# Performance work log

Hardware: AMD Instinct MI355X
Metric: run time of the kernel (lower is better)

Reference implementation:

```python
import jax, jax.numpy as jnp
import numpy as np

B, N, H, L, V = 512, 20, 450, 56, 780
T = 2 * (N - 1)  # DFS trace length per tree (down+up edge per non-root node)


def _build(rng):
    EpT = 2 * (N - 1)
    n_nodes, n_edges = B * N, B * EpT
    src = np.zeros(n_edges, np.int32); dst = np.zeros(n_edges, np.int32)
    step_eid = np.zeros((T, B), np.int32)
    step_v = np.zeros((T, B), np.int32)
    p_flag = np.zeros((T, B), np.int32)
    for b in range(B):
        par = [0] * N
        ch = [[] for _ in range(N)]
        for i in range(1, N):
            p = int(rng.integers(max(0, i - 3), i))
            par[i] = p; ch[p].append(i)
        eo, no = b * EpT, b * N
        for i in range(1, N):
            d, u = eo + 2 * (i - 1), eo + 2 * (i - 1) + 1
            src[d], dst[d] = no + par[i], no + i
            src[u], dst[u] = no + i, no + par[i]
        trace = []
        stack = [(0, iter(ch[0]))]
        while stack:
            u_, it = stack[-1]
            c = next(it, None)
            if c is None:
                stack.pop()
                if stack:
                    pu = stack[-1][0]
                    trace.append((eo + 2 * (u_ - 1) + 1, no + pu, 0))
            else:
                trace.append((eo + 2 * (c - 1), no + c, 1))
                stack.append((c, iter(ch[c])))
        for t, (e, v, p) in enumerate(trace):
            step_eid[t, b], step_v[t, b], p_flag[t, b] = e, v, p
    return src, dst, step_eid, step_v, p_flag


def setup_inputs() -> dict:
    rng = np.random.default_rng(0)
    src, dst, step_eid, step_v, p_flag = _build(rng)
    n_nodes, n_edges = B * N, B * 2 * (N - 1)
    in_lists = [[] for _ in range(n_nodes)]
    for e in range(n_edges):
        in_lists[dst[e]].append(e)
    Dn = max(len(l) for l in in_lists)
    node_in = np.full((n_nodes, Dn), n_edges, np.int32)  # pad with sentinel n_edges
    for v, l in enumerate(in_lists):
        node_in[v, :len(l)] = l
    # line-graph (non-backtracking) predecessors of edge e=(u,v): edges (w,u), w != v
    preds = [[e2 for e2 in in_lists[src[e]] if src[e2] != dst[e]] for e in range(n_edges)]
    P = max(1, max(len(l) for l in preds))
    edge_pred = np.full((n_edges, P), n_edges, np.int32)
    for e, l in enumerate(preds):
        edge_pred[e, :len(l)] = l
    wid = rng.integers(0, V, n_nodes).astype(np.int32)
    root_ids = (np.arange(B) * N).astype(np.int32)
    # q rows: root block, then per-step rows where node is new (down edges)
    q_rows = list(range(B)); q_tgt = [int(wid[r]) for r in root_ids]
    for t in range(T):
        for b in range(B):
            if p_flag[t, b]:
                q_rows.append((t + 1) * B + b)
                q_tgt.append(int(wid[step_v[t, b]]))
    p_tgt = np.concatenate([p_flag.reshape(-1), np.zeros(B, np.int32)]).astype(np.int32)
    key = jax.random.key(0)
    def W(k, *shape):
        return jax.random.normal(jax.random.fold_in(key, k), shape, jnp.float32) * 0.05
    return dict(
        tree_vec=W(0, B, L), emb=W(1, V, H),
        Wz=W(2, 2 * H, H), bz=jnp.zeros(H, jnp.float32),
        Wh=W(3, 2 * H, H), bh=jnp.zeros(H, jnp.float32),
        Wr=W(4, H, H), Ur=W(5, H, H), br=jnp.zeros(H, jnp.float32),
        Ww=W(6, H + L, H), bw=jnp.zeros(H, jnp.float32),
        Uw=W(7, 2 * H + L, H), bu=jnp.zeros(H, jnp.float32),
        Wo=W(8, H, V), bo=jnp.zeros(V, jnp.float32),
        Us=W(9, H, 1), bs=jnp.zeros(1, jnp.float32),
        wid=jnp.asarray(wid), root_ids=jnp.asarray(root_ids),
        edge_src=jnp.asarray(src), edge_dst=jnp.asarray(dst),
        edge_pred=jnp.asarray(edge_pred), node_in=jnp.asarray(node_in),
        step_eid=jnp.asarray(step_eid), step_v=jnp.asarray(step_v),
        q_rows=jnp.asarray(np.array(q_rows, np.int32)),
        q_tgt=jnp.asarray(np.array(q_tgt, np.int32)),
        p_tgt=jnp.asarray(p_tgt),
    )


def reference(tree_vec, emb, Wz, bz, Wh, bh, Wr, Ur, br, Ww, bw, Uw, bu, Wo, bo, Us, bs,
              wid, root_ids, edge_src, edge_dst, edge_pred, node_in, step_eid, step_v,
              q_rows, q_tgt, p_tgt):
    n_edges = edge_src.shape[0]
    x = emb[wid]                              # [n_nodes, H] node embeddings
    src_x = x[edge_src]; dst_x = x[edge_dst]  # [n_edges, H]
    m0 = jnp.zeros((n_edges + 1, H), x.dtype)  # +1 sentinel zero row for padding

    def step(carry, inp):
        m, rm = carry
        eid, v = inp                          # [B] edge ids / dst node ids this DFS step
        pred = edge_pred[eid]                 # [B, P] non-backtracking predecessor edges
        s = m[pred].sum(1)                    # sum of incoming m
        arm = rm[pred].sum(1)                 # sum of incoming r*m
        sx = src_x[eid]; dx = dst_x[eid]
        z = jax.nn.sigmoid(jnp.concatenate([sx, s], 1) @ Wz + bz)
        m_new = (1 - z) * s + z * jnp.tanh(jnp.concatenate([sx, arm], 1) @ Wh + bh)
        r = jax.nn.sigmoid(dx @ Wr + m_new @ Ur + br)
        m = m.at[eid].set(m_new)
        rm = rm.at[eid].set(r * m_new)
        h = m[node_in[v]].sum(1)              # node pull: h_v = sum of incoming m
        return (m, rm), h

    _, h_steps = jax.lax.scan(step, (m0, m0), (step_eid, step_v))  # [T, B, H]

    x_root = x[root_ids]
    h_root = jnp.zeros_like(x_root)           # roots pulled before any edge update
    x_steps = x[step_v]                        # [T, B, H]
    tv_steps = jnp.broadcast_to(tree_vec[None], (T, B, L))
    p_root = jnp.concatenate([x_root, h_root, tree_vec], 1)[None]
    p_step = jnp.concatenate([x_steps, h_steps, tv_steps], 2)
    p_in = jnp.concatenate([p_root, p_step], 0).reshape((T + 1) * B, 2 * H + L)
    q_root = jnp.concatenate([h_root, tree_vec], 1)[None]
    q_step = jnp.concatenate([h_steps, tv_steps], 2)
    q_in = jnp.concatenate([q_root, q_step], 0).reshape((T + 1) * B, H + L)[q_rows]

    q_logits = jax.nn.relu(q_in @ Ww + bw) @ Wo + bo          # [nq, V]
    p_logit = (jax.nn.relu(p_in @ Uw + bu) @ Us + bs)[:, 0]   # [np]
    tgt = p_tgt.astype(p_logit.dtype)
    p_loss = jnp.sum(jnp.logaddexp(0.0, p_logit) - p_logit * tgt) / B
    lse = jax.nn.logsumexp(q_logits, axis=1)
    q_loss = jnp.sum(lse - jnp.take_along_axis(q_logits, q_tgt[:, None], 1)[:, 0]) / B
    p_acc = jnp.mean(((p_logit > 0).astype(p_tgt.dtype) == p_tgt).astype(jnp.float32))
    q_acc = jnp.mean((jnp.argmax(q_logits, 1).astype(q_tgt.dtype) == q_tgt).astype(jnp.float32))
    return (q_loss, p_loss, q_acc, p_acc)
```

## Files before the change

### kernel.cpp

```cpp
#include <hip/hip_runtime.h>
#include <math.h>

#define B_ 512
#define N_ 20
#define H_ 450
#define L_ 56
#define V_ 780
#define T_ 38
#define NNODES (B_*N_)
#define NEDGES (B_*2*(N_-1))
#define NPROWS ((T_+1)*B_)
#define KS 480
#define NT 2
#define AST 488
#define HSTR 456
#define KQ 512
#define KPP 992
#define LDL 784

typedef __attribute__((ext_vector_type(8))) short bf16x8;
typedef __attribute__((ext_vector_type(4))) float f32x4;

__device__ __forceinline__ float sigmoidf_(float v){ return 1.0f/(1.0f+expf(-v)); }

__device__ __forceinline__ unsigned short f2b(float x){
  unsigned int u = __float_as_uint(x);
  unsigned int r = (u + 0x7fffu + ((u >> 16) & 1u)) >> 16;
  return (unsigned short)r;
}
__device__ __forceinline__ float b2f(unsigned int v){
  return __uint_as_float((v & 0xffffu) << 16);
}
__device__ __forceinline__ unsigned int pack2(float lo, float hi){
  return (unsigned int)f2b(lo) | ((unsigned int)f2b(hi) << 16);
}

__global__ __launch_bounds__(256) void k_gather_xb(const float* __restrict__ emb,
    const int* __restrict__ wid, unsigned short* __restrict__ xb){
  int w = blockIdx.x*4 + (threadIdx.x>>6), lane = threadIdx.x & 63;
  if (w >= NNODES) return;
  const float2* src = (const float2*)(emb + (size_t)wid[w]*H_);
  unsigned int* dst = (unsigned int*)(xb + (size_t)w*KS);
  for (int j2 = lane; j2 < 240; j2 += 64){
    unsigned int v = 0;
    if (j2 < 225){ float2 f = src[j2]; v = pack2(f.x, f.y); }
    dst[j2] = v;
  }
}

__global__ void k_wtall(const float* __restrict__ Wz, const float* __restrict__ Wh,
    const float* __restrict__ Ur, const float* __restrict__ Wr,
    const float* __restrict__ Ww, const float* __restrict__ Uw,
    const float* __restrict__ Wo, const float* __restrict__ tv,
    unsigned short* __restrict__ WzB, unsigned short* __restrict__ WhB,
    unsigned short* __restrict__ UrT, unsigned short* __restrict__ WzTop,
    unsigned short* __restrict__ WhTop, unsigned short* __restrict__ WrT,
    unsigned short* __restrict__ WwT, unsigned short* __restrict__ UwT,
    unsigned short* __restrict__ WoT, unsigned short* __restrict__ tvb){
  int bid = blockIdx.x;
  if (bid < 512*6){
    int seg = bid >> 9, c = bid & 511;
    const float* src; unsigned short* dst; int rowbase;
    switch(seg){
      case 0: src = Wz; dst = WzB; rowbase = 450; break;
      case 1: src = Wh; dst = WhB; rowbase = 450; break;
      case 2: src = Ur; dst = UrT; rowbase = 0; break;
      case 3: src = Wz; dst = WzTop; rowbase = 0; break;
      case 4: src = Wh; dst = WhTop; rowbase = 0; break;
      default: src = Wr; dst = WrT; rowbase = 0; break;
    }
    unsigned short* drow = dst + (size_t)c*KS;
    for (int k = threadIdx.x; k < KS; k += blockDim.x){
      float v = 0.f;
      if (c < 450 && k < 450) v = src[(size_t)(rowbase + k)*450 + c];
      drow[k] = f2b(v);
    }
  } else if (bid < 512*7){
    int c = bid - 512*6;
    unsigned short* drow = WwT + (size_t)c*KQ;
    for (int k = threadIdx.x; k < KQ; k += blockDim.x){
      float v = 0.f;
      if (c < 450){
        if (k < 450) v = Ww[(size_t)k*450 + c];
        else if (k >= 456) v = Ww[(size_t)(450 + k - 456)*450 + c];
      }
      drow[k] = f2b(v);
    }
  } else if (bid < 512*8){
    int c = bid - 512*7;
    unsigned short* drow = UwT + (size_t)c*KPP;
    for (int k = threadIdx.x; k < KPP; k += blockDim.x){
      float v = 0.f;
      if (c < 450){
        if (k < 450) v = Uw[(size_t)k*450 + c];
        else if (k >= 480 && k < 930) v = Uw[(size_t)(450 + k - 480)*450 + c];
        else if (k >= 936) v = Uw[(size_t)(900 + k - 936)*450 + c];
      }
      drow[k] = f2b(v);
    }
  } else if (bid < 512*8 + 832){
    int c = bid - 512*8;
    unsigned short* drow = WoT + (size_t)c*512;
    for (int k = threadIdx.x; k < 512; k += blockDim.x){
      float v = 0.f;
      if (c < V_ && k < 450) v = Wo[(size_t)k*V_ + c];
      drow[k] = f2b(v);
    }
  } else {
    int b = bid - (512*8 + 832);
    unsigned short* drow = tvb + (size_t)b*64;
    for (int k = threadIdx.x; k < 64; k += blockDim.x)
      drow[k] = f2b((k < L_) ? tv[b*L_ + k] : 0.f);
  }
}

struct ScanP {
  const unsigned short *WzB, *WhB, *UrT;
  const unsigned short *XWz, *XWh, *XWr;
  const int *edge_src, *edge_dst, *step_eid;
  unsigned short *m, *rm;
  unsigned short *hm, *hrm;
  unsigned short *hb;
};

__global__ __launch_bounds__(1024, 4) void k_scan_tree(ScanP p){
  __shared__ unsigned short A1s[16*AST];
  __shared__ unsigned short A2s[16*AST];
  __shared__ unsigned short A3s[16*AST];
  __shared__ unsigned short sZ[NT*HSTR], sH[NT*HSTR], sR[NT*HSTR];
  __shared__ int s_eoff[T_][NT], s_roff[T_][NT], s_srcH[T_][NT], s_dstH[T_][NT];

  const int tid = threadIdx.x;
  const int lane = tid & 63, l15 = lane & 15, kh = lane >> 4, ko = kh*8;
  const int wv = tid >> 6;
  const int r0 = blockIdx.x * NT;
  const int c_0 = wv*32 + l15, c_1 = c_0 + 16;

  const unsigned short* pWz0 = p.WzB + (size_t)c_0*KS;
  const unsigned short* pWz1 = p.WzB + (size_t)c_1*KS;
  const unsigned short* pWh0 = p.WhB + (size_t)c_0*KS;
  const unsigned short* pWh1 = p.WhB + (size_t)c_1*KS;
  const unsigned short* pUr0 = p.UrT + (size_t)c_0*KS;
  const unsigned short* pUr1 = p.UrT + (size_t)c_1*KS;
  const unsigned short* aA1 = A1s + l15*AST;
  const unsigned short* aA2 = A2s + l15*AST;
  const unsigned short* aA3 = A3s + l15*AST;

  for (int idx = tid; idx < 16*AST; idx += 1024){ A1s[idx] = 0; A2s[idx] = 0; A3s[idx] = 0; }
  for (int idx = tid; idx < T_*NT; idx += 1024){
    int t = idx / NT, rl = idx % NT;
    int e = p.step_eid[t*B_ + r0 + rl];
    s_eoff[t][rl] = e*KS;
    s_roff[t][rl] = (e ^ 1)*KS;
    s_srcH[t][rl] = p.edge_src[e]*HSTR;
    s_dstH[t][rl] = p.edge_dst[e]*HSTR;
  }
  __syncthreads();

  for (int t = 0; t < T_; ++t){
    bf16x8 bz0[3], bz1[3], bh0[3], bh1[3];
    #pragma unroll
    for (int i = 0; i < 3; ++i){
      bz0[i] = *(const bf16x8*)(pWz0 + i*32 + ko);
      bz1[i] = *(const bf16x8*)(pWz1 + i*32 + ko);
      bh0[i] = *(const bf16x8*)(pWh0 + i*32 + ko);
      bh1[i] = *(const bf16x8*)(pWh1 + i*32 + ko);
    }

    if (tid < NT*57){
      int rl = tid / 57, g = tid - rl*57;
      int j = g*8;
      uint4 hm4 = *(const uint4*)(p.hm  + s_srcH[t][rl] + j);
      uint4 hr4 = *(const uint4*)(p.hrm + s_srcH[t][rl] + j);
      uint4 mr4 = *(const uint4*)(p.m   + s_roff[t][rl] + j);
      uint4 rr4 = *(const uint4*)(p.rm  + s_roff[t][rl] + j);
      uint4 o1, o2;
      o1.x = pack2(b2f(hm4.x)-b2f(mr4.x), b2f(hm4.x>>16)-b2f(mr4.x>>16));
      o1.y = pack2(b2f(hm4.y)-b2f(mr4.y), b2f(hm4.y>>16)-b2f(mr4.y>>16));
      o1.z = pack2(b2f(hm4.z)-b2f(mr4.z), b2f(hm4.z>>16)-b2f(mr4.z>>16));
      o1.w = pack2(b2f(hm4.w)-b2f(mr4.w), b2f(hm4.w>>16)-b2f(mr4.w>>16));
      o2.x = pack2(b2f(hr4.x)-b2f(rr4.x), b2f(hr4.x>>16)-b2f(rr4.x>>16));
      o2.y = pack2(b2f(hr4.y)-b2f(rr4.y), b2f(hr4.y>>16)-b2f(rr4.y>>16));
      o2.z = pack2(b2f(hr4.z)-b2f(rr4.z), b2f(hr4.z>>16)-b2f(rr4.z>>16));
      o2.w = pack2(b2f(hr4.w)-b2f(rr4.w), b2f(hr4.w>>16)-b2f(rr4.w>>16));
      *(uint4*)(A1s + rl*AST + j) = o1;
      *(uint4*)(A2s + rl*AST + j) = o2;
    } else if (tid >= 128 && tid < 128 + 3*NT*57){
      int idx2 = tid - 128;
      int mat = idx2 / (NT*57), rem = idx2 - mat*(NT*57);
      int rl = rem / 57, g = rem - rl*57;
      int row = (mat == 2) ? s_dstH[t][rl] : s_srcH[t][rl];
      const unsigned short* src = (mat == 0) ? p.XWz : (mat == 1) ? p.XWh : p.XWr;
      unsigned short* d = (mat == 0) ? sZ : (mat == 1) ? sH : sR;
      *(uint4*)(d + rl*HSTR + g*8) = *(const uint4*)(src + row + g*8);
    }
    __syncthreads();

    f32x4 accZ0 = {}, accZ1 = {}, accH0 = {}, accH1 = {};
    #pragma unroll
    for (int it = 0; it < 15; ++it){
      const int sl = it % 3;
      bf16x8 a1 = *(const bf16x8*)(aA1 + it*32 + ko);
      bf16x8 a2 = *(const bf16x8*)(aA2 + it*32 + ko);
      accZ0 = __builtin_amdgcn_mfma_f32_16x16x32_bf16(a1, bz0[sl], accZ0, 0,0,0);
      accZ1 = __builtin_amdgcn_mfma_f32_16x16x32_bf16(a1, bz1[sl], accZ1, 0,0,0);
      accH0 = __builtin_amdgcn_mfma_f32_16x16x32_bf16(a2, bh0[sl], accH0, 0,0,0);
      accH1 = __builtin_amdgcn_mfma_f32_16x16x32_bf16(a2, bh1[sl], accH1, 0,0,0);
      if (it + 3 < 15){
        bz0[sl] = *(const bf16x8*)(pWz0 + (it+3)*32 + ko);
        bz1[sl] = *(const bf16x8*)(pWz1 + (it+3)*32 + ko);
        bh0[sl] = *(const bf16x8*)(pWh0 + (it+3)*32 + ko);
        bh1[sl] = *(const bf16x8*)(pWh1 + (it+3)*32 + ko);
      }
    }

    bf16x8 bu0[3], bu1[3];
    #pragma unroll
    for (int i = 0; i < 3; ++i){
      bu0[i] = *(const bf16x8*)(pUr0 + i*32 + ko);
      bu1[i] = *(const bf16x8*)(pUr1 + i*32 + ko);
    }

    if (kh == 0){
      #pragma unroll
      for (int n = 0; n < 2; ++n){
        int cc = wv*32 + n*16 + l15;
        if (cc < H_){
          f32x4 aZ = n ? accZ1 : accZ0;
          f32x4 aH = n ? accH1 : accH0;
          #pragma unroll
          for (int reg = 0; reg < NT; ++reg){
            int rl = reg;
            float z  = sigmoidf_(aZ[reg] + b2f(sZ[rl*HSTR + cc]));
            float th = tanhf   (aH[reg] + b2f(sH[rl*HSTR + cc]));
            float s_ = b2f(A1s[rl*AST + cc]);
            float mn = (1.f - z)*s_ + z*th;
            unsigned short mb = f2b(mn);
            p.m[s_eoff[t][rl] + cc] = mb;
            A3s[rl*AST + cc] = mb;
            float hv = b2f(p.hm[s_dstH[t][rl] + cc]) + mn;
            p.hm[s_dstH[t][rl] + cc] = f2b(hv);
            p.hb[(size_t)(t*B_ + r0 + rl)*HSTR + cc] = f2b(hv);
          }
        }
      }
    }
    __syncthreads();

    f32x4 accR0 = {}, accR1 = {};
    #pragma unroll
    for (int it = 0; it < 15; ++it){
      const int sl = it % 3;
      bf16x8 a = *(const bf16x8*)(aA3 + it*32 + ko);
      accR0 = __builtin_amdgcn_mfma_f32_16x16x32_bf16(a, bu0[sl], accR0, 0,0,0);
      accR1 = __builtin_amdgcn_mfma_f32_16x16x32_bf16(a, bu1[sl], accR1, 0,0,0);
      if (it + 3 < 15){
        bu0[sl] = *(const bf16x8*)(pUr0 + (it+3)*32 + ko);
        bu1[sl] = *(const bf16x8*)(pUr1 + (it+3)*32 + ko);
      }
    }

    if (kh == 0){
      #pragma unroll
      for (int n = 0; n < 2; ++n){
        int cc = wv*32 + n*16 + l15;
        if (cc < H_){
          f32x4 aR = n ? accR1 : accR0;
          #pragma unroll
          for (int reg = 0; reg < NT; ++reg){
            int rl = reg;
            float r_ = sigmoidf_(aR[reg] + b2f(sR[rl*HSTR + cc]));
            float mn = b2f(A3s[rl*AST + cc]);
            float rv = r_*mn;
            p.rm[s_eoff[t][rl] + cc] = f2b(rv);
            float hv = b2f(p.hrm[s_dstH[t][rl] + cc]) + rv;
            p.hrm[s_dstH[t][rl] + cc] = f2b(hv);
          }
        }
      }
    }
    __syncthreads();
  }
}

__global__ __launch_bounds__(256) void k_head_mfma(
    const unsigned short* __restrict__ A, const unsigned short* __restrict__ BT, int K,
    const float* __restrict__ bias, int Nact, int relu,
    float* __restrict__ outF, int ldF, unsigned short* __restrict__ outB, int ldB)
{
  __shared__ unsigned short As[64*40], Bs[64*40];
  const int tid = threadIdx.x;
  const int gr0 = blockIdx.y*64, gc0 = blockIdx.x*64;
  const int lane = tid & 63;
  const int w = tid >> 6, wr = w >> 1, wc = w & 1;
  const int l15 = lane & 15, kh = lane >> 4;
  const int sr = tid >> 2, sj = (tid & 3) * 8;
  f32x4 acc[2][2] = {};
  for (int kt = 0; kt < K; kt += 32){
    __syncthreads();
    *(float4*)&As[sr*40 + sj] = *(const float4*)&A[(size_t)(gr0+sr)*K + kt + sj];
    *(float4*)&Bs[sr*40 + sj] = *(const float4*)&BT[(size_t)(gc0+sr)*K + kt + sj];
    __syncthreads();
    bf16x8 a0 = *(const bf16x8*)&As[(wr*32      + l15)*40 + kh*8];
    bf16x8 a1 = *(const bf16x8*)&As[(wr*32 + 16 + l15)*40 + kh*8];
    bf16x8 b0 = *(const bf16x8*)&Bs[(wc*32      + l15)*40 + kh*8];
    bf16x8 b1 = *(const bf16x8*)&Bs[(wc*32 + 16 + l15)*40 + kh*8];
    acc[0][0] = __builtin_amdgcn_mfma_f32_16x16x32_bf16(a0,b0,acc[0][0],0,0,0);
    acc[0][1] = __builtin_amdgcn_mfma_f32_16x16x32_bf16(a0,b1,acc[0][1],0,0,0);
    acc[1][0] = __builtin_amdgcn_mfma_f32_16x16x32_bf16(a1,b0,acc[1][0],0,0,0);
    acc[1][1] = __builtin_amdgcn_mfma_f32_16x16x32_bf16(a1,b1,acc[1][1],0,0,0);
  }
  #pragma unroll
  for (int mi = 0; mi < 2; ++mi){
    #pragma unroll
    for (int n = 0; n < 2; ++n){
      int c = gc0 + wc*32 + n*16 + l15;
      float bc = (c < Nact) ? bias[c] : 0.f;
      #pragma unroll
      for (int reg = 0; reg < 4; ++reg){
        int r = gr0 + wr*32 + mi*16 + kh*4 + reg;
        float v = acc[mi][n][reg] + bc;
        if (relu) v = fmaxf(v, 0.f);
        if (outF && c < Nact) outF[(size_t)r*ldF + c] = v;
        if (outB && c < ldB)  outB[(size_t)r*ldB + c] = (c < Nact) ? f2b(v) : (unsigned short)0;
      }
    }
  }
}

__global__ __launch_bounds__(256) void k_xw(const unsigned short* __restrict__ xb,
    const unsigned short* __restrict__ WzTop, const unsigned short* __restrict__ WhTop,
    const unsigned short* __restrict__ WrT,
    const float* __restrict__ bz, const float* __restrict__ bh, const float* __restrict__ br,
    unsigned short* __restrict__ XWz, unsigned short* __restrict__ XWh,
    unsigned short* __restrict__ XWr)
{
  __shared__ unsigned short As[64*40], Bs[64*40];
  const unsigned short* BT = (blockIdx.z == 0) ? WzTop : (blockIdx.z == 1) ? WhTop : WrT;
  const float* bias        = (blockIdx.z == 0) ? bz    : (blockIdx.z == 1) ? bh    : br;
  unsigned short* outB     = (blockIdx.z == 0) ? XWz   : (blockIdx.z == 1) ? XWh   : XWr;
  const int tid = threadIdx.x;
  const int gr0 = blockIdx.y*64, gc0 = blockIdx.x*64;
  const int lane = tid & 63;
  const int w = tid >> 6, wr = w >> 1, wc = w & 1;
  const int l15 = lane & 15, kh = lane >> 4;
  const int sr = tid >> 2, sj = (tid & 3) * 8;
  f32x4 acc[2][2] = {};
  for (int kt = 0; kt < KS; kt += 32){
    __syncthreads();
    *(float4*)&As[sr*40 + sj] = *(const float4*)&xb[(size_t)(gr0+sr)*KS + kt + sj];
    *(float4*)&Bs[sr*40 + sj] = *(const float4*)&BT[(size_t)(gc0+sr)*KS + kt + sj];
    __syncthreads();
    bf16x8 a0 = *(const bf16x8*)&As[(wr*32      + l15)*40 + kh*8];
    bf16x8 a1 = *(const bf16x8*)&As[(wr*32 + 16 + l15)*40 + kh*8];
    bf16x8 b0 = *(const bf16x8*)&Bs[(wc*32      + l15)*40 + kh*8];
// ... 183 lines not shown
      int tg = q_tgt[i];
      float lt = b2f((unsigned int)logits[(size_t)i*LDL + tg]);
      qloss += mx + logf(ps) - lt;
      qacc  += (mi == tg) ? 1.f : 0.f;
    }
  }
  if (lane == 0){
    atomicAdd(out+0, qloss*(1.0f/B_));
    atomicAdd(out+2, qacc *(1.0f/(float)nq));
  }
}

__global__ __launch_bounds__(256) void k_pfinal(const float* __restrict__ plog,
    const float* __restrict__ bs, const int* __restrict__ p_tgt, float* __restrict__ out){
  int i = blockIdx.x*256 + threadIdx.x;
  float loss = 0.f, acc = 0.f;
  if (i < NPROWS){
    float pl = plog[i] + bs[0];
    float tgt = (float)p_tgt[i];
    loss = fmaxf(pl, 0.f) + log1pf(expf(-fabsf(pl))) - pl*tgt;
    acc = (((pl > 0.f) ? 1 : 0) == p_tgt[i]) ? 1.f : 0.f;
  }
  #pragma unroll
  for (int off = 32; off; off >>= 1){
    loss += __shfl_xor(loss, off); acc += __shfl_xor(acc, off);
  }
  if ((threadIdx.x & 63) == 0){
    atomicAdd(out+1, loss*(1.0f/B_));
    atomicAdd(out+3, acc *(1.0f/(float)NPROWS));
  }
}

extern "C" void kernel_launch(void* const* d_in, const int* in_sizes, int n_in,
                              void* d_out, int out_size, void* d_ws, size_t ws_size,
                              hipStream_t stream){
  const float* tree_vec = (const float*)d_in[0];
  const float* emb  = (const float*)d_in[1];
  const float* Wz   = (const float*)d_in[2];
  const float* bz   = (const float*)d_in[3];
  const float* Wh   = (const float*)d_in[4];
  const float* bh   = (const float*)d_in[5];
  const float* Wr   = (const float*)d_in[6];
  const float* Ur   = (const float*)d_in[7];
  const float* br   = (const float*)d_in[8];
  const float* Ww   = (const float*)d_in[9];
  const float* bw   = (const float*)d_in[10];
  const float* Uw   = (const float*)d_in[11];
  const float* bu   = (const float*)d_in[12];
  const float* Wo   = (const float*)d_in[13];
  const float* bo   = (const float*)d_in[14];
  const float* Us   = (const float*)d_in[15];
  const float* bs   = (const float*)d_in[16];
  const int* wid      = (const int*)d_in[17];
  const int* root_ids = (const int*)d_in[18];
  const int* edge_src = (const int*)d_in[19];
  const int* edge_dst = (const int*)d_in[20];
  const int* step_eid = (const int*)d_in[23];
  const int* step_v   = (const int*)d_in[24];
  const int* q_rows   = (const int*)d_in[25];
  const int* q_tgt    = (const int*)d_in[26];
  const int* p_tgt    = (const int*)d_in[27];
  int nq = in_sizes[25];

  char* ws = (char*)d_ws;
  const size_t XB_OFF    = 0;
  const size_t HB_OFF    = 9830400;
  const size_t M_OFF     = 27574272;
  const size_t RM_OFF    = M_OFF + 18678784;
  const size_t HM_OFF    = RM_OFF + 18678784;
  const size_t HRM_OFF   = HM_OFF + 9338880;
  const size_t WZB_OFF   = HRM_OFF + 9338880;
  const size_t WHB_OFF   = WZB_OFF + 491520;
  const size_t URT_OFF   = WHB_OFF + 491520;
  const size_t WZTOP_OFF = URT_OFF + 491520;
  const size_t WHTOP_OFF = WZTOP_OFF + 491520;
  const size_t WRT_OFF   = WHTOP_OFF + 491520;
  const size_t WWT_OFF   = WRT_OFF + 491520;
  const size_t UWT_OFF   = WWT_OFF + 524288;
  const size_t WOT_OFF   = UWT_OFF + 1015808;
  const size_t TVB_OFF   = WOT_OFF + 851968;
  const size_t XWZ_OFF   = TVB_OFF + 65536;
  const size_t XWH_OFF   = XWZ_OFF + 9338880;
  const size_t XWR_OFF   = XWH_OFF + 9338880;
  const size_t LQ_OFF  = M_OFF;
  const size_t HQB_OFF = XWZ_OFF;
  const size_t PL_OFF  = XWH_OFF;

  unsigned short* xb = (unsigned short*)(ws + XB_OFF);
  unsigned short* hb = (unsigned short*)(ws + HB_OFF);
  unsigned short* m_ = (unsigned short*)(ws + M_OFF);
  unsigned short* rm = (unsigned short*)(ws + RM_OFF);
  unsigned short* hm = (unsigned short*)(ws + HM_OFF);
  unsigned short* hrm = (unsigned short*)(ws + HRM_OFF);
  unsigned short* WzB = (unsigned short*)(ws + WZB_OFF);
  unsigned short* WhB = (unsigned short*)(ws + WHB_OFF);
  unsigned short* UrT = (unsigned short*)(ws + URT_OFF);
  unsigned short* WzTop = (unsigned short*)(ws + WZTOP_OFF);
  unsigned short* WhTop = (unsigned short*)(ws + WHTOP_OFF);
  unsigned short* WrT = (unsigned short*)(ws + WRT_OFF);
  unsigned short* WwT = (unsigned short*)(ws + WWT_OFF);
  unsigned short* UwT = (unsigned short*)(ws + UWT_OFF);
  unsigned short* WoT = (unsigned short*)(ws + WOT_OFF);
  unsigned short* tvb = (unsigned short*)(ws + TVB_OFF);
  unsigned short* XWz = (unsigned short*)(ws + XWZ_OFF);
  unsigned short* XWh = (unsigned short*)(ws + XWH_OFF);
  unsigned short* XWr = (unsigned short*)(ws + XWR_OFF);

  hipMemsetAsync(ws + M_OFF, 0, 2*18678784ull + 2*9338880ull, stream);
  hipMemsetAsync(d_out, 0, (size_t)out_size*sizeof(float), stream);

  k_gather_xb<<<2560, 256, 0, stream>>>(emb, wid, xb);
  k_wtall<<<512*8 + 832 + 512, 256, 0, stream>>>(Wz, Wh, Ur, Wr, Ww, Uw, Wo, tree_vec,
      WzB, WhB, UrT, WzTop, WhTop, WrT, WwT, UwT, WoT, tvb);
  k_xw<<<dim3(8,160,3), 256, 0, stream>>>(xb, WzTop, WhTop, WrT, bz, bh, br, XWz, XWh, XWr);

  ScanP sp;
  sp.WzB = WzB; sp.WhB = WhB; sp.UrT = UrT;
  sp.XWz = XWz; sp.XWh = XWh; sp.XWr = XWr;
  sp.edge_src = edge_src; sp.edge_dst = edge_dst; sp.step_eid = step_eid;
  sp.m = m_; sp.rm = rm; sp.hm = hm; sp.hrm = hrm; sp.hb = hb;
  k_scan_tree<<<B_/NT, 1024, 0, stream>>>(sp);

  unsigned short* logitsq = (unsigned short*)(ws + LQ_OFF);
  unsigned short* hqb     = (unsigned short*)(ws + HQB_OFF);
  float* plog             = (float*)(ws + PL_OFF);
  hipMemsetAsync(plog, 0, (size_t)NPROWS*4, stream);

  k_head_q<<<dim3(8, nq/64), 256, 0, stream>>>(hb, tvb, q_rows, WwT, bw, hqb, nq);
  k_head_mfma<<<dim3(13, nq/64), 256, 0, stream>>>(hqb, WoT, 512, bo, V_, 0,
      nullptr, 0, logitsq, LDL);
  k_qreduce3<<<320, 256, 0, stream>>>(logitsq, q_tgt, nq, (float*)d_out);

  k_head_p2<<<dim3(8, NPROWS/64), 256, 0, stream>>>(xb, hb, tvb, root_ids, step_v,
      UwT, bu, Us, plog);
  k_pfinal<<<78, 256, 0, stream>>>(plog, bs, p_tgt, (float*)d_out);
}
```

Baseline: 1.200 ms.

## Swizzle LDS A-tiles, split gather across more threads, skip idle wave

Pads the LDS A-tile row stride to 512 and XOR-swizzles column offsets by row, so the MFMA A-fragment reads avoid bank conflicts. The hm/m gather now uses 228 threads with 8-byte loads instead of 114 threads with 16-byte loads, and the XW row copy moves to threads starting at 256. The 16th wave, whose columns fall past H, no longer loads weights or issues MFMAs. The swizzle must match in the writer and every reader, and padded rows that stay zero depend on where the XOR lands.

```diff
diff --git a/kernel.cpp b/kernel.cpp
--- a/kernel.cpp
+++ b/kernel.cpp
@@ -12,7 +12,7 @@
 #define NPROWS ((T_+1)*B_)
 #define KS 480
 #define NT 2
-#define AST 488
+#define AST 512
 #define HSTR 456
 #define KQ 512
 #define KPP 992
@@ -135,6 +135,8 @@
   const int wv = tid >> 6;
   const int r0 = blockIdx.x * NT;
   const int c_0 = wv*32 + l15, c_1 = c_0 + 16;
+  const int sw = (l15 & 7) << 3;
+  const bool act = (wv < 15);
 
   const unsigned short* pWz0 = p.WzB + (size_t)c_0*KS;
   const unsigned short* pWz1 = p.WzB + (size_t)c_1*KS;
@@ -159,34 +161,33 @@
 
   for (int t = 0; t < T_; ++t){
     bf16x8 bz0[3], bz1[3], bh0[3], bh1[3];
-    #pragma unroll
-    for (int i = 0; i < 3; ++i){
-      bz0[i] = *(const bf16x8*)(pWz0 + i*32 + ko);
-      bz1[i] = *(const bf16x8*)(pWz1 + i*32 + ko);
-      bh0[i] = *(const bf16x8*)(pWh0 + i*32 + ko);
-      bh1[i] = *(const bf16x8*)(pWh1 + i*32 + ko);
-    }
-
-    if (tid < NT*57){
-      int rl = tid / 57, g = tid - rl*57;
-      int j = g*8;
-      uint4 hm4 = *(const uint4*)(p.hm  + s_srcH[t][rl] + j);
-      uint4 hr4 = *(const uint4*)(p.hrm + s_srcH[t][rl] + j);
-      uint4 mr4 = *(const uint4*)(p.m   + s_roff[t][rl] + j);
-      uint4 rr4 = *(const uint4*)(p.rm  + s_roff[t][rl] + j);
-      uint4 o1, o2;
-      o1.x = pack2(b2f(hm4.x)-b2f(mr4.x), b2f(hm4.x>>16)-b2f(mr4.x>>16));
-      o1.y = pack2(b2f(hm4.y)-b2f(mr4.y), b2f(hm4.y>>16)-b2f(mr4.y>>16));
-      o1.z = pack2(b2f(hm4.z)-b2f(mr4.z), b2f(hm4.z>>16)-b2f(mr4.z>>16));
-      o1.w = pack2(b2f(hm4.w)-b2f(mr4.w), b2f(hm4.w>>16)-b2f(mr4.w>>16));
-      o2.x = pack2(b2f(hr4.x)-b2f(rr4.x), b2f(hr4.x>>16)-b2f(rr4.x>>16));
-      o2.y = pack2(b2f(hr4.y)-b2f(rr4.y), b2f(hr4.y>>16)-b2f(rr4.y>>16));
-      o2.z = pack2(b2f(hr4.z)-b2f(rr4.z), b2f(hr4.z>>16)-b2f(rr4.z>>16));
-      o2.w = pack2(b2f(hr4.w)-b2f(rr4.w), b2f(hr4.w>>16)-b2f(rr4.w>>16));
-      *(uint4*)(A1s + rl*AST + j) = o1;
-      *(uint4*)(A2s + rl*AST + j) = o2;
-    } else if (tid >= 128 && tid < 128 + 3*NT*57){
-      int idx2 = tid - 128;
+    if (act){
+      #pragma unroll
+      for (int i = 0; i < 3; ++i){
+        bz0[i] = *(const bf16x8*)(pWz0 + i*32 + ko);
+        bz1[i] = *(const bf16x8*)(pWz1 + i*32 + ko);
+        bh0[i] = *(const bf16x8*)(pWh0 + i*32 + ko);
+        bh1[i] = *(const bf16x8*)(pWh1 + i*32 + ko);
+      }
+    }
+
+    if (tid < NT*114){
+      int rl = tid / 114, g = tid - rl*114;
+      int j = g*4;
+      uint2 hm2 = *(const uint2*)(p.hm  + s_srcH[t][rl] + j);
+      uint2 hr2 = *(const uint2*)(p.hrm + s_srcH[t][rl] + j);
+      uint2 mr2 = *(const uint2*)(p.m   + s_roff[t][rl] + j);
+      uint2 rr2 = *(const uint2*)(p.rm  + s_roff[t][rl] + j);
+      uint2 o1, o2;
+      o1.x = pack2(b2f(hm2.x)-b2f(mr2.x), b2f(hm2.x>>16)-b2f(mr2.x>>16));
+      o1.y = pack2(b2f(hm2.y)-b2f(mr2.y), b2f(hm2.y>>16)-b2f(mr2.y>>16));
+      o2.x = pack2(b2f(hr2.x)-b2f(rr2.x), b2f(hr2.x>>16)-b2f(rr2.x>>16));
+      o2.y = pack2(b2f(hr2.y)-b2f(rr2.y), b2f(hr2.y>>16)-b2f(rr2.y>>16));
+      int so = j ^ ((rl & 7) << 3);
+      *(uint2*)(A1s + rl*AST + so) = o1;
+      *(uint2*)(A2s + rl*AST + so) = o2;
+    } else if (tid >= 256 && tid < 256 + 3*NT*57){
+      int idx2 = tid - 256;
       int mat = idx2 / (NT*57), rem = idx2 - mat*(NT*57);
       int rl = rem / 57, g = rem - rl*57;
       int row = (mat == 2) ? s_dstH[t][rl] : s_srcH[t][rl];
@@ -197,28 +198,33 @@
     __syncthreads();
 
     f32x4 accZ0 = {}, accZ1 = {}, accH0 = {}, accH1 = {};
-    #pragma unroll
-    for (int it = 0; it < 15; ++it){
-      const int sl = it % 3;
-      bf16x8 a1 = *(const bf16x8*)(aA1 + it*32 + ko);
-      bf16x8 a2 = *(const bf16x8*)(aA2 + it*32 + ko);
-      accZ0 = __builtin_amdgcn_mfma_f32_16x16x32_bf16(a1, bz0[sl], accZ0, 0,0,0);
-      accZ1 = __builtin_amdgcn_mfma_f32_16x16x32_bf16(a1, bz1[sl], accZ1, 0,0,0);
-      accH0 = __builtin_amdgcn_mfma_f32_16x16x32_bf16(a2, bh0[sl], accH0, 0,0,0);
-      accH1 = __builtin_amdgcn_mfma_f32_16x16x32_bf16(a2, bh1[sl], accH1, 0,0,0);
-      if (it + 3 < 15){
-        bz0[sl] = *(const bf16x8*)(pWz0 + (it+3)*32 + ko);
-        bz1[sl] = *(const bf16x8*)(pWz1 + (it+3)*32 + ko);
-        bh0[sl] = *(const bf16x8*)(pWh0 + (it+3)*32 + ko);
-        bh1[sl] = *(const bf16x8*)(pWh1 + (it+3)*32 + ko);
+    if (act){
+      #pragma unroll
+      for (int it = 0; it < 15; ++it){
+        const int sl = it % 3;
+        const int so = (it*32 + ko) ^ sw;
+        bf16x8 a1 = *(const bf16x8*)(aA1 + so);
+        bf16x8 a2 = *(const bf16x8*)(aA2 + so);
+        accZ0 = __builtin_amdgcn_mfma_f32_16x16x32_bf16(a1, bz0[sl], accZ0, 0,0,0);
+        accZ1 = __builtin_amdgcn_mfma_f32_16x16x32_bf16(a1, bz1[sl], accZ1, 0,0,0);
+        accH0 = __builtin_amdgcn_mfma_f32_16x16x32_bf16(a2, bh0[sl], accH0, 0,0,0);
+        accH1 = __builtin_amdgcn_mfma_f32_16x16x32_bf16(a2, bh1[sl], accH1, 0,0,0);
+        if (it + 3 < 15){
+          bz0[sl] = *(const bf16x8*)(pWz0 + (it+3)*32 + ko);
+          bz1[sl] = *(const bf16x8*)(pWz1 + (it+3)*32 + ko);
+          bh0[sl] = *(const bf16x8*)(pWh0 + (it+3)*32 + ko);
+          bh1[sl] = *(const bf16x8*)(pWh1 + (it+3)*32 + ko);
+        }
       }
     }
 
     bf16x8 bu0[3], bu1[3];
-    #pragma unroll
-    for (int i = 0; i < 3; ++i){
-      bu0[i] = *(const bf16x8*)(pUr0 + i*32 + ko);
-      bu1[i] = *(const bf16x8*)(pUr1 + i*32 + ko);
+    if (act){
+      #pragma unroll
+      for (int i = 0; i < 3; ++i){
+        bu0[i] = *(const bf16x8*)(pUr0 + i*32 + ko);
+        bu1[i] = *(const bf16x8*)(pUr1 + i*32 + ko);
+      }
     }
 
     if (kh == 0){
@@ -231,13 +237,14 @@
           #pragma unroll
           for (int reg = 0; reg < NT; ++reg){
             int rl = reg;
+            int so = cc ^ ((rl & 7) << 3);
             float z  = sigmoidf_(aZ[reg] + b2f(sZ[rl*HSTR + cc]));
             float th = tanhf   (aH[reg] + b2f(sH[rl*HSTR + cc]));
-            float s_ = b2f(A1s[rl*AST + cc]);
+            float s_ = b2f(A1s[rl*AST + so]);
             float mn = (1.f - z)*s_ + z*th;
             unsigned short mb = f2b(mn);
             p.m[s_eoff[t][rl] + cc] = mb;
-            A3s[rl*AST + cc] = mb;
+            A3s[rl*AST + so] = mb;
             float hv = b2f(p.hm[s_dstH[t][rl] + cc]) + mn;
             p.hm[s_dstH[t][rl] + cc] = f2b(hv);
             p.hb[(size_t)(t*B_ + r0 + rl)*HSTR + cc] = f2b(hv);
@@ -248,15 +255,17 @@
     __syncthreads();
 
     f32x4 accR0 = {}, accR1 = {};
-    #pragma unroll
-    for (int it = 0; it < 15; ++it){
-      const int sl = it % 3;
-      bf16x8 a = *(const bf16x8*)(aA3 + it*32 + ko);
-      accR0 = __builtin_amdgcn_mfma_f32_16x16x32_bf16(a, bu0[sl], accR0, 0,0,0);
-      accR1 = __builtin_amdgcn_mfma_f32_16x16x32_bf16(a, bu1[sl], accR1, 0,0,0);
-      if (it + 3 < 15){
-        bu0[sl] = *(const bf16x8*)(pUr0 + (it+3)*32 + ko);
-        bu1[sl] = *(const bf16x8*)(pUr1 + (it+3)*32 + ko);
+    if (act){
+      #pragma unroll
+      for (int it = 0; it < 15; ++it){
+        const int sl = it % 3;
+        bf16x8 a = *(const bf16x8*)(aA3 + ((it*32 + ko) ^ sw));
+        accR0 = __builtin_amdgcn_mfma_f32_16x16x32_bf16(a, bu0[sl], accR0, 0,0,0);
+        accR1 = __builtin_amdgcn_mfma_f32_16x16x32_bf16(a, bu1[sl], accR1, 0,0,0);
+        if (it + 3 < 15){
+          bu0[sl] = *(const bf16x8*)(pUr0 + (it+3)*32 + ko);
+          bu1[sl] = *(const bf16x8*)(pUr1 + (it+3)*32 + ko);
+        }
       }
     }
 
@@ -269,8 +278,9 @@
           #pragma unroll
           for (int reg = 0; reg < NT; ++reg){
             int rl = reg;
+            int so = cc ^ ((rl & 7) << 3);
             float r_ = sigmoidf_(aR[reg] + b2f(sR[rl*HSTR + cc]));
-            float mn = b2f(A3s[rl*AST + cc]);
+            float mn = b2f(A3s[rl*AST + so]);
             float rv = r_*mn;
             p.rm[s_eoff[t][rl] + cc] = f2b(rv);
             float hv = b2f(p.hrm[s_dstH[t][rl] + cc]) + rv;
```

After: 1.554 ms. 1.3x slower.

## Quantize tree-scan recurrent GEMMs to FP8 e4m3 with scaled weights

Applied to the files above, without the earlier changes.

The recurrent matmuls in the sequential tree scan move from bf16 MFMA to fp8 e4m3 MFMA. Weights are pre-quantized with a scale of 16, and activations are quantized to fp8 in shared memory using a permuted layout, which halves weight and LDS traffic per step. A bf16 copy of the message difference is kept for the gating arithmetic. The r-gate now reads m back from global memory instead of shared. This risks accuracy loss from e4m3 rounding of both activations and weights inside a recurrence.

```diff
diff --git a/kernel.cpp b/kernel.cpp
--- a/kernel.cpp
+++ b/kernel.cpp
@@ -12,7 +12,7 @@
 #define NPROWS ((T_+1)*B_)
 #define KS 480
 #define NT 2
-#define AST 488
+#define ASTQ 528
 #define HSTR 456
 #define KQ 512
 #define KPP 992
@@ -20,6 +20,7 @@
 
 typedef __attribute__((ext_vector_type(8))) short bf16x8;
 typedef __attribute__((ext_vector_type(4))) float f32x4;
+typedef __attribute__((ext_vector_type(2))) long i64x2;
 
 __device__ __forceinline__ float sigmoidf_(float v){ return 1.0f/(1.0f+expf(-v)); }
 
@@ -33,6 +34,26 @@
 }
 __device__ __forceinline__ unsigned int pack2(float lo, float hi){
   return (unsigned int)f2b(lo) | ((unsigned int)f2b(hi) << 16);
+}
+__device__ __forceinline__ unsigned char f2e4m3(float x){
+  unsigned int u = __float_as_uint(x);
+  unsigned char sgn = (u >> 24) & 0x80;
+  unsigned int au = u & 0x7fffffffu;
+  if (au >= 0x43e00000u) return sgn | 0x7e;
+  if (au < 0x3c800000u){
+    float t = __uint_as_float(au) * 512.f;
+    int q = (int)rintf(t);
+    if (q >= 8) return sgn | 0x08;
+    return sgn | (unsigned char)q;
+  }
+  unsigned int r = au + 0x7ffffu + ((au >> 20) & 1u);
+  if (r >= 0x43e00000u) return sgn | 0x7e;
+  int e = (int)((r >> 23) & 0xff) - 120;
+  unsigned int m = (r >> 20) & 7u;
+  return sgn | (unsigned char)((e << 3) | m);
+}
+__device__ __forceinline__ int foff_(int k){
+  return ((k >> 3) & 3)*128 + (k >> 5)*8 + (k & 7);
 }
 
 __global__ __launch_bounds__(256) void k_gather_xb(const float* __restrict__ emb,
@@ -114,8 +135,19 @@
   }
 }
 
+__global__ void k_wt8(const float* __restrict__ W, int Kact, int Nact,
+                      unsigned char* __restrict__ dst){
+  int c = blockIdx.x;
+  unsigned char* drow = dst + (size_t)c*512;
+  for (int k = threadIdx.x; k < 512; k += blockDim.x){
+    float v = 0.f;
+    if (c < Nact && k < Kact) v = W[(size_t)k*Nact + c] * 16.f;
+    drow[foff_(k)] = f2e4m3(v);
+  }
+}
+
 struct ScanP {
-  const unsigned short *WzB, *WhB, *UrT;
+  const unsigned char *WzQ, *WhQ, *UrQ;
   const unsigned short *XWz, *XWh, *XWr;
   const int *edge_src, *edge_dst, *step_eid;
   unsigned short *m, *rm;
@@ -124,29 +156,33 @@
 };
 
 __global__ __launch_bounds__(1024, 4) void k_scan_tree(ScanP p){
-  __shared__ unsigned short A1s[16*AST];
-  __shared__ unsigned short A2s[16*AST];
-  __shared__ unsigned short A3s[16*AST];
+  __shared__ unsigned char A1s[16*ASTQ];
+  __shared__ unsigned char A2s[16*ASTQ];
+  __shared__ unsigned char A3s[16*ASTQ];
+  __shared__ unsigned short SLb[NT*HSTR];
   __shared__ unsigned short sZ[NT*HSTR], sH[NT*HSTR], sR[NT*HSTR];
   __shared__ int s_eoff[T_][NT], s_roff[T_][NT], s_srcH[T_][NT], s_dstH[T_][NT];
 
   const int tid = threadIdx.x;
-  const int lane = tid & 63, l15 = lane & 15, kh = lane >> 4, ko = kh*8;
+  const int lane = tid & 63, l15 = lane & 15, kh = lane >> 4;
   const int wv = tid >> 6;
   const int r0 = blockIdx.x * NT;
   const int c_0 = wv*32 + l15, c_1 = c_0 + 16;
 
-  const unsigned short* pWz0 = p.WzB + (size_t)c_0*KS;
-  const unsigned short* pWz1 = p.WzB + (size_t)c_1*KS;
-  const unsigned short* pWh0 = p.WhB + (size_t)c_0*KS;
-  const unsigned short* pWh1 = p.WhB + (size_t)c_1*KS;
-  const unsigned short* pUr0 = p.UrT + (size_t)c_0*KS;
-  const unsigned short* pUr1 = p.UrT + (size_t)c_1*KS;
-  const unsigned short* aA1 = A1s + l15*AST;
-  const unsigned short* aA2 = A2s + l15*AST;
-  const unsigned short* aA3 = A3s + l15*AST;
-
-  for (int idx = tid; idx < 16*AST; idx += 1024){ A1s[idx] = 0; A2s[idx] = 0; A3s[idx] = 0; }
+  const unsigned char* qWz0 = p.WzQ + (size_t)c_0*512 + kh*128;
+  const unsigned char* qWz1 = p.WzQ + (size_t)c_1*512 + kh*128;
+  const unsigned char* qWh0 = p.WhQ + (size_t)c_0*512 + kh*128;
+  const unsigned char* qWh1 = p.WhQ + (size_t)c_1*512 + kh*128;
+  const unsigned char* qUr0 = p.UrQ + (size_t)c_0*512 + kh*128;
+  const unsigned char* qUr1 = p.UrQ + (size_t)c_1*512 + kh*128;
+  const unsigned char* aA1q = A1s + l15*ASTQ + kh*128;
+  const unsigned char* aA2q = A2s + l15*ASTQ + kh*128;
+  const unsigned char* aA3q = A3s + l15*ASTQ + kh*128;
+
+  for (int idx = tid; idx < 16*ASTQ/4; idx += 1024){
+    ((unsigned int*)A1s)[idx] = 0u; ((unsigned int*)A2s)[idx] = 0u;
+    ((unsigned int*)A3s)[idx] = 0u;
+  }
   for (int idx = tid; idx < T_*NT; idx += 1024){
     int t = idx / NT, rl = idx % NT;
     int e = p.step_eid[t*B_ + r0 + rl];
@@ -158,13 +194,13 @@
   __syncthreads();
 
   for (int t = 0; t < T_; ++t){
-    bf16x8 bz0[3], bz1[3], bh0[3], bh1[3];
+    i64x2 rz0[3], rz1[3], rh0[3], rh1[3];
     #pragma unroll
     for (int i = 0; i < 3; ++i){
-      bz0[i] = *(const bf16x8*)(pWz0 + i*32 + ko);
-      bz1[i] = *(const bf16x8*)(pWz1 + i*32 + ko);
-      bh0[i] = *(const bf16x8*)(pWh0 + i*32 + ko);
-      bh1[i] = *(const bf16x8*)(pWh1 + i*32 + ko);
+      rz0[i] = *(const i64x2*)(qWz0 + i*16);
+      rz1[i] = *(const i64x2*)(qWz1 + i*16);
+      rh0[i] = *(const i64x2*)(qWh0 + i*16);
+      rh1[i] = *(const i64x2*)(qWh1 + i*16);
     }
 
     if (tid < NT*57){
@@ -174,17 +210,24 @@
       uint4 hr4 = *(const uint4*)(p.hrm + s_srcH[t][rl] + j);
       uint4 mr4 = *(const uint4*)(p.m   + s_roff[t][rl] + j);
       uint4 rr4 = *(const uint4*)(p.rm  + s_roff[t][rl] + j);
-      uint4 o1, o2;
-      o1.x = pack2(b2f(hm4.x)-b2f(mr4.x), b2f(hm4.x>>16)-b2f(mr4.x>>16));
-      o1.y = pack2(b2f(hm4.y)-b2f(mr4.y), b2f(hm4.y>>16)-b2f(mr4.y>>16));
-      o1.z = pack2(b2f(hm4.z)-b2f(mr4.z), b2f(hm4.z>>16)-b2f(mr4.z>>16));
-      o1.w = pack2(b2f(hm4.w)-b2f(mr4.w), b2f(hm4.w>>16)-b2f(mr4.w>>16));
-      o2.x = pack2(b2f(hr4.x)-b2f(rr4.x), b2f(hr4.x>>16)-b2f(rr4.x>>16));
-      o2.y = pack2(b2f(hr4.y)-b2f(rr4.y), b2f(hr4.y>>16)-b2f(rr4.y>>16));
-      o2.z = pack2(b2f(hr4.z)-b2f(rr4.z), b2f(hr4.z>>16)-b2f(rr4.z>>16));
-      o2.w = pack2(b2f(hr4.w)-b2f(rr4.w), b2f(hr4.w>>16)-b2f(rr4.w>>16));
-      *(uint4*)(A1s + rl*AST + j) = o1;
-      *(uint4*)(A2s + rl*AST + j) = o2;
+      float f0 = b2f(hm4.x)-b2f(mr4.x), f1 = b2f(hm4.x>>16)-b2f(mr4.x>>16);
+      float f2 = b2f(hm4.y)-b2f(mr4.y), f3 = b2f(hm4.y>>16)-b2f(mr4.y>>16);
+      float f4 = b2f(hm4.z)-b2f(mr4.z), f5 = b2f(hm4.z>>16)-b2f(mr4.z>>16);
+      float f6 = b2f(hm4.w)-b2f(mr4.w), f7 = b2f(hm4.w>>16)-b2f(mr4.w>>16);
+      float a0 = b2f(hr4.x)-b2f(rr4.x), a1 = b2f(hr4.x>>16)-b2f(rr4.x>>16);
+      float a2 = b2f(hr4.y)-b2f(rr4.y), a3 = b2f(hr4.y>>16)-b2f(rr4.y>>16);
+      float a4 = b2f(hr4.z)-b2f(rr4.z), a5 = b2f(hr4.z>>16)-b2f(rr4.z>>16);
+      float a6 = b2f(hr4.w)-b2f(rr4.w), a7 = b2f(hr4.w>>16)-b2f(rr4.w>>16);
+      int fo = ((j>>3)&3)*128 + (j>>5)*8;
+      uint2 w1, w2;
+      w1.x = (unsigned)f2e4m3(f0) | ((unsigned)f2e4m3(f1)<<8) | ((unsigned)f2e4m3(f2)<<16) | ((unsigned)f2e4m3(f3)<<24);
+      w1.y = (unsigned)f2e4m3(f4) | ((unsigned)f2e4m3(f5)<<8) | ((unsigned)f2e4m3(f6)<<16) | ((unsigned)f2e4m3(f7)<<24);
+      w2.x = (unsigned)f2e4m3(a0) | ((unsigned)f2e4m3(a1)<<8) | ((unsigned)f2e4m3(a2)<<16) | ((unsigned)f2e4m3(a3)<<24);
+      w2.y = (unsigned)f2e4m3(a4) | ((unsigned)f2e4m3(a5)<<8) | ((unsigned)f2e4m3(a6)<<16) | ((unsigned)f2e4m3(a7)<<24);
+      *(uint2*)(A1s + rl*ASTQ + fo) = w1;
+      *(uint2*)(A2s + rl*ASTQ + fo) = w2;
+      uint4 sb; sb.x = pack2(f0,f1); sb.y = pack2(f2,f3); sb.z = pack2(f4,f5); sb.w = pack2(f6,f7);
+      *(uint4*)(SLb + rl*HSTR + j) = sb;
     } else if (tid >= 128 && tid < 128 + 3*NT*57){
       int idx2 = tid - 128;
       int mat = idx2 / (NT*57), rem = idx2 - mat*(NT*57);
@@ -198,27 +241,31 @@
 
     f32x4 accZ0 = {}, accZ1 = {}, accH0 = {}, accH1 = {};
     #pragma unroll
-    for (int it = 0; it < 15; ++it){
-      const int sl = it % 3;
-      bf16x8 a1 = *(const bf16x8*)(aA1 + it*32 + ko);
-      bf16x8 a2 = *(const bf16x8*)(aA2 + it*32 + ko);
-      accZ0 = __builtin_amdgcn_mfma_f32_16x16x32_bf16(a1, bz0[sl], accZ0, 0,0,0);
-      accZ1 = __builtin_amdgcn_mfma_f32_16x16x32_bf16(a1, bz1[sl], accZ1, 0,0,0);
-      accH0 = __builtin_amdgcn_mfma_f32_16x16x32_bf16(a2, bh0[sl], accH0, 0,0,0);
-      accH1 = __builtin_amdgcn_mfma_f32_16x16x32_bf16(a2, bh1[sl], accH1, 0,0,0);
-      if (it + 3 < 15){
-        bz0[sl] = *(const bf16x8*)(pWz0 + (it+3)*32 + ko);
-        bz1[sl] = *(const bf16x8*)(pWz1 + (it+3)*32 + ko);
-        bh0[sl] = *(const bf16x8*)(pWh0 + (it+3)*32 + ko);
-        bh1[sl] = *(const bf16x8*)(pWh1 + (it+3)*32 + ko);
-      }
-    }
-
-    bf16x8 bu0[3], bu1[3];
+    for (int c = 0; c < 8; ++c){
+      const int sl = c % 3;
+      i64x2 a1 = *(const i64x2*)(aA1q + c*16);
+      i64x2 a2 = *(const i64x2*)(aA2q + c*16);
+      accZ0 = __builtin_amdgcn_mfma_f32_16x16x32_fp8_fp8(a1.x, rz0[sl].x, accZ0, 0,0,0);
+      accZ0 = __builtin_amdgcn_mfma_f32_16x16x32_fp8_fp8(a1.y, rz0[sl].y, accZ0, 0,0,0);
+      accZ1 = __builtin_amdgcn_mfma_f32_16x16x32_fp8_fp8(a1.x, rz1[sl].x, accZ1, 0,0,0);
+      accZ1 = __builtin_amdgcn_mfma_f32_16x16x32_fp8_fp8(a1.y, rz1[sl].y, accZ1, 0,0,0);
+      accH0 = __builtin_amdgcn_mfma_f32_16x16x32_fp8_fp8(a2.x, rh0[sl].x, accH0, 0,0,0);
+      accH0 = __builtin_amdgcn_mfma_f32_16x16x32_fp8_fp8(a2.y, rh0[sl].y, accH0, 0,0,0);
+      accH1 = __builtin_amdgcn_mfma_f32_16x16x32_fp8_fp8(a2.x, rh1[sl].x, accH1, 0,0,0);
+      accH1 = __builtin_amdgcn_mfma_f32_16x16x32_fp8_fp8(a2.y, rh1[sl].y, accH1, 0,0,0);
+      if (c < 5){
+        rz0[sl] = *(const i64x2*)(qWz0 + (c+3)*16);
+        rz1[sl] = *(const i64x2*)(qWz1 + (c+3)*16);
+        rh0[sl] = *(const i64x2*)(qWh0 + (c+3)*16);
+        rh1[sl] = *(const i64x2*)(qWh1 + (c+3)*16);
+      }
+    }
+
+    i64x2 ru0[3], ru1[3];
     #pragma unroll
     for (int i = 0; i < 3; ++i){
-      bu0[i] = *(const bf16x8*)(pUr0 + i*32 + ko);
-      bu1[i] = *(const bf16x8*)(pUr1 + i*32 + ko);
+      ru0[i] = *(const i64x2*)(qUr0 + i*16);
+      ru1[i] = *(const i64x2*)(qUr1 + i*16);
     }
 
     if (kh == 0){
@@ -231,13 +278,12 @@
           #pragma unroll
           for (int reg = 0; reg < NT; ++reg){
             int rl = reg;
-            float z  = sigmoidf_(aZ[reg] + b2f(sZ[rl*HSTR + cc]));
-            float th = tanhf   (aH[reg] + b2f(sH[rl*HSTR + cc]));
-            float s_ = b2f(A1s[rl*AST + cc]);
+            float z  = sigmoidf_(aZ[reg]*0.0625f + b2f(sZ[rl*HSTR + cc]));
+            float th = tanhf   (aH[reg]*0.0625f + b2f(sH[rl*HSTR + cc]));
+            float s_ = b2f(SLb[rl*HSTR + cc]);
             float mn = (1.f - z)*s_ + z*th;
-            unsigned short mb = f2b(mn);
-            p.m[s_eoff[t][rl] + cc] = mb;
-            A3s[rl*AST + cc] = mb;
+            p.m[s_eoff[t][rl] + cc] = f2b(mn);
+            A3s[rl*ASTQ + foff_(cc)] = f2e4m3(mn);
             float hv = b2f(p.hm[s_dstH[t][rl] + cc]) + mn;
             p.hm[s_dstH[t][rl] + cc] = f2b(hv);
             p.hb[(size_t)(t*B_ + r0 + rl)*HSTR + cc] = f2b(hv);
@@ -249,14 +295,16 @@
 
     f32x4 accR0 = {}, accR1 = {};
     #pragma unroll
-    for (int it = 0; it < 15; ++it){
-      const int sl = it % 3;
-      bf16x8 a = *(const bf16x8*)(aA3 + it*32 + ko);
-      accR0 = __builtin_amdgcn_mfma_f32_16x16x32_bf16(a, bu0[sl], accR0, 0,0,0);
-      accR1 = __builtin_amdgcn_mfma_f32_16x16x32_bf16(a, bu1[sl], accR1, 0,0,0);
-      if (it + 3 < 15){
-        bu0[sl] = *(const bf16x8*)(pUr0 + (it+3)*32 + ko);
-        bu1[sl] = *(const bf16x8*)(pUr1 + (it+3)*32 + ko);
+    for (int c = 0; c < 8; ++c){
+      const int sl = c % 3;
+      i64x2 a = *(const i64x2*)(aA3q + c*16);
+      accR0 = __builtin_amdgcn_mfma_f32_16x16x32_fp8_fp8(a.x, ru0[sl].x, accR0, 0,0,0);
+      accR0 = __builtin_amdgcn_mfma_f32_16x16x32_fp8_fp8(a.y, ru0[sl].y, accR0, 0,0,0);
+      accR1 = __builtin_amdgcn_mfma_f32_16x16x32_fp8_fp8(a.x, ru1[sl].x, accR1, 0,0,0);
+      accR1 = __builtin_amdgcn_mfma_f32_16x16x32_fp8_fp8(a.y, ru1[sl].y, accR1, 0,0,0);
+      if (c < 5){
+        ru0[sl] = *(const i64x2*)(qUr0 + (c+3)*16);
+        ru1[sl] = *(const i64x2*)(qUr1 + (c+3)*16);
       }
     }
 
@@ -269,8 +317,8 @@
           #pragma unroll
           for (int reg = 0; reg < NT; ++reg){
             int rl = reg;
-            float r_ = sigmoidf_(aR[reg] + b2f(sR[rl*HSTR + cc]));
-            float mn = b2f(A3s[rl*AST + cc]);
+            float r_ = sigmoidf_(aR[reg]*0.0625f + b2f(sR[rl*HSTR + cc]));
+            float mn = b2f(p.m[s_eoff[t][rl] + cc]);
             float rv = r_*mn;
             p.rm[s_eoff[t][rl] + cc] = f2b(rv);
             float hv = b2f(p.hrm[s_dstH[t][rl] + cc]) + rv;
@@ -620,6 +668,9 @@
   const size_t XWZ_OFF   = TVB_OFF + 65536;
   const size_t XWH_OFF   = XWZ_OFF + 9338880;
   const size_t XWR_OFF   = XWH_OFF + 9338880;
+  const size_t WZQ_OFF   = XWR_OFF + 9338880;
+  const size_t WHQ_OFF   = WZQ_OFF + 262144;
+  const size_t URQ_OFF   = WHQ_OFF + 262144;
   const size_t LQ_OFF  = M_OFF;
   const size_t HQB_OFF = XWZ_OFF;
   const size_t PL_OFF  = XWH_OFF;
@@ -643,6 +694,9 @@
   unsigned short* XWz = (unsigned short*)(ws + XWZ_OFF);
   unsigned short* XWh = (unsigned short*)(ws + XWH_OFF);
   unsigned short* XWr = (unsigned short*)(ws + XWR_OFF);
+  unsigned char* WzQ = (unsigned char*)(ws + WZQ_OFF);
+  unsigned char* WhQ = (unsigned char*)(ws + WHQ_OFF);
+  unsigned char* UrQ = (unsigned char*)(ws + URQ_OFF);
 
   hipMemsetAsync(ws + M_OFF, 0, 2*18678784ull + 2*9338880ull, stream);
   hipMemsetAsync(d_out, 0, (size_t)out_size*sizeof(float), stream);
@@ -650,10 +704,13 @@
   k_gather_xb<<<2560, 256, 0, stream>>>(emb, wid, xb);
   k_wtall<<<512*8 + 832 + 512, 256, 0, stream>>>(Wz, Wh, Ur, Wr, Ww, Uw, Wo, tree_vec,
       WzB, WhB, UrT, WzTop, WhTop, WrT, WwT, UwT, WoT, tvb);
+  k_wt8<<<512, 256, 0, stream>>>(Wz + 450*450, 450, 450, WzQ);
+  k_wt8<<<512, 256, 0, stream>>>(Wh + 450*450, 450, 450, WhQ);
+  k_wt8<<<512, 256, 0, stream>>>(Ur, 450, 450, UrQ);
   k_xw<<<dim3(8,160,3), 256, 0, stream>>>(xb, WzTop, WhTop, WrT, bz, bh, br, XWz, XWh, XWr);
 
   ScanP sp;
-  sp.WzB = WzB; sp.WhB = WhB; sp.UrT = UrT;
+  sp.WzQ = WzQ; sp.WhQ = WhQ; sp.UrQ = UrQ;
   sp.XWz = XWz; sp.XWh = XWh; sp.XWr = XWr;
   sp.edge_src = edge_src; sp.edge_dst = edge_dst; sp.step_eid = step_eid;
   sp.m = m_; sp.rm = rm; sp.hm = hm; sp.hrm = hrm; sp.hb = hb;
```

After: 1.717 ms. 43.1% more time.
